# Kernel tuning notes

Hardware: AMD Instinct MI355X
Metric: run time of the kernel (lower is better)

The kernel has to match this reference:

```python
import jax, jax.numpy as jnp
import numpy as np

B, N, MODEL_D = 2, 1024, 2048
KQ_D, V_D, H, I = 128, 128, 8, 4
ROPE_THETA = 10000.0


def _rope(x, theta):
    # x: [b, n, ..., d]; positions along axis 1, rotation over last dim d.
    d = x.shape[-1]
    n = x.shape[1]
    inv_freq = theta ** (-jnp.arange(0, d, 2, dtype=jnp.float32) / d)  # [d/2]
    ang = jnp.arange(n, dtype=jnp.float32)[:, None] * inv_freq          # [n, d/2]
    bshape = (1, n) + (1,) * (x.ndim - 3) + (d // 2,)
    cos = jnp.cos(ang).reshape(bshape).astype(x.dtype)
    sin = jnp.sin(ang).reshape(bshape).astype(x.dtype)
    x1, x2 = jnp.split(x, 2, axis=-1)
    return jnp.concatenate([x1 * cos - x2 * sin, x1 * sin + x2 * cos], axis=-1)


def setup_inputs() -> dict:
    key = jax.random.key(0)
    kx, kq, kk, kv, ko = jax.random.split(key, 5)
    s_in = 1.0 / np.sqrt(MODEL_D)
    s_out = 1.0 / np.sqrt(H * I * V_D)
    x = jax.random.normal(kx, (B, N, MODEL_D), jnp.float32)
    Wq = jax.random.normal(kq, (MODEL_D, H, I, KQ_D), jnp.float32) * s_in
    Wk = jax.random.normal(kk, (MODEL_D, H, KQ_D), jnp.float32) * s_in
    Wv = jax.random.normal(kv, (MODEL_D, H, V_D), jnp.float32) * s_in
    Wo = jax.random.normal(ko, (H, I, V_D, MODEL_D), jnp.float32) * s_out
    return {"x": x, "Wq": Wq, "Wk": Wk, "Wv": Wv, "Wo": Wo}


def reference(x, Wq, Wk, Wv, Wo):
    # GQA projections (per Ueajsum specs)
    q = jnp.einsum('bnd,dhik->bnhik', x, Wq)   # [B,N,H,I,K]
    k = jnp.einsum('bnd,dhc->bnhc', x, Wk)     # [B,N,H,K]
    v = jnp.einsum('bnd,dhv->bnhv', x, Wv)     # [B,N,H,V]
    # RoPE on q and k
    q = _rope(q, ROPE_THETA)
    k = _rope(k, ROPE_THETA)
    # Causal softmax attention, each kv head serves I query heads
    scale = 1.0 / np.sqrt(KQ_D)
    scores = jnp.einsum('bnhic,bmhc->bhinm', q, k) * scale  # [B,H,I,N,N]
    n = x.shape[1]
    causal = jnp.tril(jnp.ones((n, n), dtype=bool))
    scores = jnp.where(causal, scores, jnp.finfo(scores.dtype).min)
    p = jax.nn.softmax(scores, axis=-1)
    out = jnp.einsum('bhinm,bmhv->bnhiv', p, v)              # [B,N,H,I,V]
    return jnp.einsum('bnhiv,hivd->bnd', out, Wo)            # [B,N,D]
```

## Files before the change

### kernel.cpp

```cpp
#include <hip/hip_runtime.h>
#include <hip/hip_bf16.h>

typedef __bf16 bf16x8 __attribute__((ext_vector_type(8)));
typedef float floatx4 __attribute__((ext_vector_type(4)));

static __device__ __forceinline__ void async_cp16(const __bf16* g, __bf16* l) {
    typedef const __attribute__((address_space(1))) unsigned int gu32;
    typedef __attribute__((address_space(3))) unsigned int lu32;
    __builtin_amdgcn_global_load_lds((gu32*)g, (lu32*)l, 16, 0, 0);
}

__global__ __launch_bounds__(256) void prep_kernel(
    const float* __restrict__ x,  __bf16* __restrict__ xb,
    const float* __restrict__ Wq, const float* __restrict__ Wk,
    const float* __restrict__ Wv, __bf16* __restrict__ Wt)
{
    __shared__ float tile[32][33];
    const int bk  = blockIdx.x;
    const int tid = threadIdx.x;
    const int tx  = tid & 31, ty = tid >> 5;

    if (bk < 12288) {
        const float* src; __bf16* dst; int R = 2048, C; int bxx, byy;
        if (bk < 8192)        { src = Wq; dst = Wt;                          C = 4096; bxx = bk & 127;           byy = bk >> 7; }
        else if (bk < 10240)  { src = Wk; dst = Wt + (size_t)4096 * 2048;    C = 1024; bxx = (bk - 8192) & 31;   byy = (bk - 8192) >> 5; }
        else                  { src = Wv; dst = Wt + (size_t)5120 * 2048;    C = 1024; bxx = (bk - 10240) & 31;  byy = (bk - 10240) >> 5; }
        const int c0 = bxx * 32, r0 = byy * 32;
        #pragma unroll
        for (int j = 0; j < 4; ++j)
            tile[ty * 4 + j][tx] = src[(size_t)(r0 + ty * 4 + j) * C + c0 + tx];
        __syncthreads();
        #pragma unroll
        for (int j = 0; j < 4; ++j)
            dst[(size_t)(c0 + ty * 4 + j) * R + r0 + tx] = (__bf16)tile[tx][ty * 4 + j];
    } else {
        int idx = (bk - 12288) * 256 + tid;
        const float* p = x + (size_t)idx * 8;
        float4 f0 = *(const float4*)p;
        float4 f1 = *(const float4*)(p + 4);
        union { uint4 u; __bf16 b[8]; } o;
        o.b[0] = (__bf16)f0.x; o.b[1] = (__bf16)f0.y; o.b[2] = (__bf16)f0.z; o.b[3] = (__bf16)f0.w;
        o.b[4] = (__bf16)f1.x; o.b[5] = (__bf16)f1.y; o.b[6] = (__bf16)f1.z; o.b[7] = (__bf16)f1.w;
        *(uint4*)(xb + (size_t)idx * 8) = o.u;
    }
}

__global__ void transpose_cvt_kernel(const float* __restrict__ src,
                                     __bf16* __restrict__ dst, int R, int C)
{
    __shared__ float tile[32][33];
    const int tx = threadIdx.x, ty = threadIdx.y;
    const int c0 = blockIdx.x * 32, r0 = blockIdx.y * 32;
    #pragma unroll
    for (int j = 0; j < 4; ++j)
        tile[ty * 4 + j][tx] = src[(size_t)(r0 + ty * 4 + j) * C + c0 + tx];
    __syncthreads();
    #pragma unroll
    for (int j = 0; j < 4; ++j)
        dst[(size_t)(c0 + ty * 4 + j) * R + r0 + tx] = (__bf16)tile[tx][ty * 4 + j];
}

__global__ __launch_bounds__(256) void rope_vtrans_kernel(
    __bf16* __restrict__ qkv, __bf16* __restrict__ vt)
{
    __shared__ __bf16 tile[32][33];
    const int bk  = blockIdx.x;
    const int tid = threadIdx.x;

    if (bk < 2560) {
        int idx  = bk * 256 + tid;
        int part = idx & 7;
        int t    = idx >> 3;
        int head = t % 40;
        int row  = t / 40;
        int n    = row & 1023;
        int col0 = (head < 32) ? head * 128 : 4096 + (head - 32) * 128;
        size_t base = (size_t)row * 6144 + col0 + part * 8;

        union { uint4 u; __bf16 b[8]; } x1, x2, o1, o2;
        x1.u = *(const uint4*)(qkv + base);
        x2.u = *(const uint4*)(qkv + base + 64);
        #pragma unroll
        for (int e = 0; e < 8; ++e) {
            int j = part * 8 + e;
            float inv_freq = exp2f(-(float)j * 0.20762050593046015f);
            float ang = (float)n * inv_freq;
            float sv, cv;
            __sincosf(ang, &sv, &cv);
            float a = (float)x1.b[e], b2 = (float)x2.b[e];
            o1.b[e] = (__bf16)(a * cv - b2 * sv);
            o2.b[e] = (__bf16)(a * sv + b2 * cv);
        }
        *(uint4*)(qkv + base)      = o1.u;
        *(uint4*)(qkv + base + 64) = o2.u;
    } else {
        int idx = bk - 2560;
        const int tx = tid & 31, ty = tid >> 5;
        const int k0 = (idx & 31) * 32;
        const int v0 = ((idx >> 5) & 3) * 32;
        const int bh = idx >> 7;
        const int b = bh >> 3, h = bh & 7;
        #pragma unroll
        for (int j = 0; j < 4; ++j)
            tile[ty * 4 + j][tx] =
                qkv[(size_t)(b * 1024 + k0 + ty * 4 + j) * 6144 + 5120 + h * 128 + v0 + tx];
        __syncthreads();
        #pragma unroll
        for (int j = 0; j < 4; ++j)
            vt[((size_t)bh * 128 + v0 + ty * 4 + j) * 1024 + k0 + tx] = tile[tx][ty * 4 + j];
    }
}

template <typename TC>
__global__ __launch_bounds__(256) void gemm_bt(
    const __bf16* __restrict__ A,
    const __bf16* __restrict__ Bt,
    TC* __restrict__ C,
    int M, int N, int Kc, int lda, int ldb, int ldc)
{
    __shared__ __bf16 As[128 * 32];
    __shared__ __bf16 Bs[128 * 32];

    const int tid  = threadIdx.x;
    const int wave = tid >> 6;
    const int lane = tid & 63;
    const int quad = lane >> 4;
    const int l15  = lane & 15;
    const int wr   = wave >> 1, wc = wave & 1;

    const int bm = blockIdx.y * 128;
    const int bn = blockIdx.x * 128;
    const int z  = blockIdx.z;

    A  += (size_t)z * Kc;
    Bt += (size_t)z * Kc;
    C  += (size_t)z * M * ldc;

    floatx4 acc[16];
    #pragma unroll
    for (int i = 0; i < 16; ++i) acc[i] = floatx4{0.f, 0.f, 0.f, 0.f};

    const __bf16* a0 = A  + (size_t)(bm + wave * 32 + (lane >> 2)) * lda + (lane & 3) * 8;
    const __bf16* b0 = Bt + (size_t)(bn + wave * 32 + (lane >> 2)) * ldb + (lane & 3) * 8;
    __bf16* asd0 = As + (wave * 32) * 32;
    __bf16* asd1 = As + (wave * 32 + 16) * 32;
    __bf16* bsd0 = Bs + (wave * 32) * 32;
    __bf16* bsd1 = Bs + (wave * 32 + 16) * 32;

    for (int k0 = 0; k0 < Kc; k0 += 32) {
        __syncthreads();
        async_cp16(a0 + k0,                    asd0);
        async_cp16(a0 + (size_t)16 * lda + k0, asd1);
        async_cp16(b0 + k0,                    bsd0);
        async_cp16(b0 + (size_t)16 * ldb + k0, bsd1);
        __syncthreads();

        bf16x8 af[4], bf[4];
        #pragma unroll
        for (int t = 0; t < 4; ++t)
            af[t] = *(const bf16x8*)(&As[(wr * 64 + t * 16 + l15) * 32 + quad * 8]);
        #pragma unroll
        for (int u = 0; u < 4; ++u)
            bf[u] = *(const bf16x8*)(&Bs[(wc * 64 + u * 16 + l15) * 32 + quad * 8]);
        #pragma unroll
        for (int t = 0; t < 4; ++t)
            #pragma unroll
            for (int u = 0; u < 4; ++u)
                acc[t * 4 + u] = __builtin_amdgcn_mfma_f32_16x16x32_bf16(
                    af[t], bf[u], acc[t * 4 + u], 0, 0, 0);
    }

    #pragma unroll
    for (int t = 0; t < 4; ++t)
        #pragma unroll
        for (int u = 0; u < 4; ++u)
            #pragma unroll
            for (int r = 0; r < 4; ++r) {
                int row = bm + wr * 64 + t * 16 + quad * 4 + r;
                int col = bn + wc * 64 + u * 16 + l15;
                C[(size_t)row * ldc + col] = (TC)acc[t * 4 + u][r];
            }
}

__global__ __launch_bounds__(256) void reduce_kernel(
    const __bf16* __restrict__ part, float* __restrict__ out)
{
    int idx = blockIdx.x * 256 + threadIdx.x;
    const size_t STRIDE = (size_t)2048 * 2048;
    union { uint4 u; __bf16 b[8]; } p0, p1;
    p0.u = *(const uint4*)(part + (size_t)idx * 8);
    p1.u = *(const uint4*)(part + STRIDE + (size_t)idx * 8);
    float4 o0, o1;
    o0.x = (float)p0.b[0] + (float)p1.b[0];
    o0.y = (float)p0.b[1] + (float)p1.b[1];
    o0.z = (float)p0.b[2] + (float)p1.b[2];
    o0.w = (float)p0.b[3] + (float)p1.b[3];
    o1.x = (float)p0.b[4] + (float)p1.b[4];
    o1.y = (float)p0.b[5] + (float)p1.b[5];
    o1.z = (float)p0.b[6] + (float)p1.b[6];
    o1.w = (float)p0.b[7] + (float)p1.b[7];
    *(float4*)(out + (size_t)idx * 8)     = o0;
    *(float4*)(out + (size_t)idx * 8 + 4) = o1;
}

__global__ __launch_bounds__(512, 2) void attn_kernel(
    const __bf16* __restrict__ qkv,
    const __bf16* __restrict__ vt,
    __bf16* __restrict__ ao)
{
    const int PS_LD = 72;
    __shared__ __bf16 Ks[64 * 128];
    __shared__ __bf16 Vs[128 * 64];
    __shared__ __bf16 Ps[8][16 * PS_LD];

    const int tid  = threadIdx.x;
    const int wave = tid >> 6;
    const int lane = tid & 63;
    const int quad = lane >> 4;
    const int l15  = lane & 15;
    const int i    = wave >> 1;
    const int rt   = wave & 1;

    const int pair = blockIdx.x;
    const int bh   = blockIdx.y;
    const int b    = bh >> 3, h = bh & 7;
    const __bf16* vtb = vt + (size_t)bh * 128 * 1024;

    const int keyA = wave * 8 + (lane >> 4);
    const int keyB = keyA + 4;
    const int chA  = (lane & 15) ^ (keyA & 15);
    const int chB  = (lane & 15) ^ (keyB & 15);
    const __bf16* gK0 = qkv + (size_t)(b * 1024 + keyA) * 6144 + 4096 + h * 128 + chA * 8;
    const __bf16* gK1 = qkv + (size_t)(b * 1024 + keyB) * 6144 + 4096 + h * 128 + chB * 8;
    __bf16* lK0 = Ks + (wave * 8) * 128;
    __bf16* lK1 = Ks + (wave * 8 + 4) * 128;

    const int vdA = wave * 16 + (lane >> 3);
    const int vdB = vdA + 8;
    const int cvA = (lane & 7) ^ (vdA & 7);
    const int cvB = (lane & 7) ^ (vdB & 7);
    const __bf16* gV0 = vtb + (size_t)vdA * 1024 + cvA * 8;
    const __bf16* gV1 = vtb + (size_t)vdB * 1024 + cvB * 8;
    __bf16* lV0 = Vs + (wave * 16) * 64;
    __bf16* lV1 = Vs + (wave * 16 + 8) * 64;

    bf16x8 onesf;
    #pragma unroll
    for (int j = 0; j < 8; ++j) onesf[j] = (__bf16)1.0f;

    const float C2 = 0.12751898549f;

    #pragma unroll
    for (int ph = 0; ph < 2; ++ph) {
        const int qt    = ph ? (31 - pair) : pair;
        const int qrow0 = qt * 32 + rt * 16;

        const __bf16* qp = qkv + (size_t)(b * 1024 + qrow0 + l15) * 6144 + (h * 4 + i) * 128;
        bf16x8 qf[4];
        #pragma unroll
        for (int c = 0; c < 4; ++c)
            qf[c] = *(const bf16x8*)(qp + c * 32 + quad * 8);

        floatx4 acc[8];
        #pragma unroll
        for (int u = 0; u < 8; ++u) acc[u] = floatx4{0.f, 0.f, 0.f, 0.f};
        floatx4 accl = floatx4{0.f, 0.f, 0.f, 0.f};

        const int ntiles = (qt >> 1) + 1;
        for (int t = 0; t < ntiles; ++t) {
            const int kt = t * 64;
            __syncthreads();
            async_cp16(gK0 + (size_t)kt * 6144, lK0);
            async_cp16(gK1 + (size_t)kt * 6144, lK1);
            async_cp16(gV0 + kt, lV0);
            async_cp16(gV1 + kt, lV1);
            __syncthreads();

            floatx4 s[4];
            #pragma unroll
            for (int ks = 0; ks < 4; ++ks) s[ks] = floatx4{0.f, 0.f, 0.f, 0.f};
            #pragma unroll
            for (int c = 0; c < 4; ++c) {
                #pragma unroll
                for (int ks = 0; ks < 4; ++ks) {
                    bf16x8 kf = *(const bf16x8*)(
                        &Ks[(ks * 16 + l15) * 128 + ((c * 4 + quad) ^ l15) * 8]);
                    s[ks] = __builtin_amdgcn_mfma_f32_16x16x32_bf16(qf[c], kf, s[ks], 0, 0, 0);
                }
            }

            #pragma unroll
            for (int r = 0; r < 4; ++r) {
                int qrow = qrow0 + quad * 4 + r;
                #pragma unroll
                for (int ks = 0; ks < 4; ++ks) {
                    int kc = kt + ks * 16 + l15;
                    float p = (kc <= qrow) ? exp2f(s[ks][r] * C2) : 0.0f;
                    Ps[wave][(quad * 4 + r) * PS_LD + ks * 16 + l15] = (__bf16)p;
                }
            }

            #pragma unroll
            for (int s2 = 0; s2 < 2; ++s2) {
                bf16x8 pa = *(const bf16x8*)(&Ps[wave][l15 * PS_LD + s2 * 32 + quad * 8]);
                accl = __builtin_amdgcn_mfma_f32_16x16x32_bf16(pa, onesf, accl, 0, 0, 0);
                #pragma unroll
                for (int u = 0; u < 8; ++u) {
                    bf16x8 vf = *(const bf16x8*)(
                        &Vs[(u * 16 + l15) * 64 + (((s2 * 4 + quad) ^ (l15 & 7))) * 8]);
                    acc[u] = __builtin_amdgcn_mfma_f32_16x16x32_bf16(pa, vf, acc[u], 0, 0, 0);
                }
            }
        }

        #pragma unroll
        for (int r = 0; r < 4; ++r) {
            float inv = 1.0f / accl[r];
            int row = qrow0 + quad * 4 + r;
            __bf16* op = ao + (size_t)(b * 1024 + row) * 4096 + (h * 4 + i) * 128;
            #pragma unroll
            for (int u = 0; u < 8; ++u)
                op[u * 16 + l15] = (__bf16)(acc[u][r] * inv);
        }
    }
}

extern "C" void kernel_launch(void* const* d_in, const int* in_sizes, int n_in,
                              void* d_out, int out_size, void* d_ws, size_t ws_size,
                              hipStream_t stream)
{
    const float* x  = (const float*)d_in[0];
    const float* Wq = (const float*)d_in[1];
    const float* Wk = (const float*)d_in[2];
    const float* Wv = (const float*)d_in[3];
    const float* Wo = (const float*)d_in[4];
    float* out = (float*)d_out;

    const size_t MB = 1024 * 1024;
    char* ws = (char*)d_ws;
    __bf16* qkv  = (__bf16*)(ws);
    __bf16* vtb  = (__bf16*)(ws + 24 * MB);
    __bf16* xb   = (__bf16*)(ws + 28 * MB);
    __bf16* Wt   = (__bf16*)(ws + 36 * MB);
    __bf16* ao   = (__bf16*)(ws + 28 * MB);
    __bf16* WoT  = (__bf16*)(ws + 44 * MB);
    __bf16* part = (__bf16*)(ws);

    prep_kernel<<<14336, 256, 0, stream>>>(x, xb, Wq, Wk, Wv, Wt);
    gemm_bt<__bf16><<<dim3(48, 16), 256, 0, stream>>>(xb, Wt, qkv, 2048, 6144, 2048, 2048, 2048, 6144);
    transpose_cvt_kernel<<<dim3(64, 128), dim3(32, 8), 0, stream>>>(Wo, WoT, 4096, 2048);
    rope_vtrans_kernel<<<4608, 256, 0, stream>>>(qkv, vtb);
    attn_kernel<<<dim3(16, 16), 512, 0, stream>>>(qkv, vtb, ao);
    gemm_bt<__bf16><<<dim3(16, 16, 2), 256, 0, stream>>>(ao, WoT, part, 2048, 2048, 2048, 4096, 4096, 2048);
    reduce_kernel<<<2048, 256, 0, stream>>>(part, out);
}
```

Before: 323.5 us.

## Use swizzled 64-wide K tiles in GEMM, 3-way split-K, fuse Wo transpose

The GEMM now stages 64-wide K slices per sync, using an XOR swizzle on LDS columns to avoid bank conflicts. This halves the number of barrier pairs per K and doubles the MFMA work per load phase. The output projection switches from a 2-way to an uneven 3-way split-K (1344/1344/1408) for more blocks and better CU occupancy, with the reduce kernel summing three partials. The Wo transpose/convert is folded into the rope/V-transpose launch to remove one kernel launch. LDS use per block doubles, and the extra partial adds memory traffic in the reduce step.

```diff
diff --git a/kernel.cpp b/kernel.cpp
--- a/kernel.cpp
+++ b/kernel.cpp
@@ -45,25 +45,12 @@
     }
 }
 
-__global__ void transpose_cvt_kernel(const float* __restrict__ src,
-                                     __bf16* __restrict__ dst, int R, int C)
-{
-    __shared__ float tile[32][33];
-    const int tx = threadIdx.x, ty = threadIdx.y;
-    const int c0 = blockIdx.x * 32, r0 = blockIdx.y * 32;
-    #pragma unroll
-    for (int j = 0; j < 4; ++j)
-        tile[ty * 4 + j][tx] = src[(size_t)(r0 + ty * 4 + j) * C + c0 + tx];
-    __syncthreads();
-    #pragma unroll
-    for (int j = 0; j < 4; ++j)
-        dst[(size_t)(c0 + ty * 4 + j) * R + r0 + tx] = (__bf16)tile[tx][ty * 4 + j];
-}
-
-__global__ __launch_bounds__(256) void rope_vtrans_kernel(
-    __bf16* __restrict__ qkv, __bf16* __restrict__ vt)
-{
-    __shared__ __bf16 tile[32][33];
+__global__ __launch_bounds__(256) void rope_vtrans_wot_kernel(
+    __bf16* __restrict__ qkv, __bf16* __restrict__ vt,
+    const float* __restrict__ Wo, __bf16* __restrict__ WoT)
+{
+    __shared__ float tilef[32][33];
+    __shared__ __bf16 tileb[32][33];
     const int bk  = blockIdx.x;
     const int tid = threadIdx.x;
 
@@ -93,7 +80,7 @@
         }
         *(uint4*)(qkv + base)      = o1.u;
         *(uint4*)(qkv + base + 64) = o2.u;
-    } else {
+    } else if (bk < 4608) {
         int idx = bk - 2560;
         const int tx = tid & 31, ty = tid >> 5;
         const int k0 = (idx & 31) * 32;
@@ -102,24 +89,36 @@
         const int b = bh >> 3, h = bh & 7;
         #pragma unroll
         for (int j = 0; j < 4; ++j)
-            tile[ty * 4 + j][tx] =
+            tileb[ty * 4 + j][tx] =
                 qkv[(size_t)(b * 1024 + k0 + ty * 4 + j) * 6144 + 5120 + h * 128 + v0 + tx];
         __syncthreads();
         #pragma unroll
         for (int j = 0; j < 4; ++j)
-            vt[((size_t)bh * 128 + v0 + ty * 4 + j) * 1024 + k0 + tx] = tile[tx][ty * 4 + j];
+            vt[((size_t)bh * 128 + v0 + ty * 4 + j) * 1024 + k0 + tx] = tileb[tx][ty * 4 + j];
+    } else {
+        int idx = bk - 4608;
+        const int tx = tid & 31, ty = tid >> 5;
+        const int c0 = (idx & 63) * 32;
+        const int r0 = (idx >> 6) * 32;
+        #pragma unroll
+        for (int j = 0; j < 4; ++j)
+            tilef[ty * 4 + j][tx] = Wo[(size_t)(r0 + ty * 4 + j) * 2048 + c0 + tx];
+        __syncthreads();
+        #pragma unroll
+        for (int j = 0; j < 4; ++j)
+            WoT[(size_t)(c0 + ty * 4 + j) * 4096 + r0 + tx] = (__bf16)tilef[tx][ty * 4 + j];
     }
 }
 
-template <typename TC>
 __global__ __launch_bounds__(256) void gemm_bt(
     const __bf16* __restrict__ A,
     const __bf16* __restrict__ Bt,
-    TC* __restrict__ C,
-    int M, int N, int Kc, int lda, int ldb, int ldc)
-{
-    __shared__ __bf16 As[128 * 32];
-    __shared__ __bf16 Bs[128 * 32];
+    __bf16* __restrict__ C,
+    int M, int lda, int ldb, int ldc,
+    int kc_base, int kc_extra)
+{
+    __shared__ __bf16 As[128 * 64];
+    __shared__ __bf16 Bs[128 * 64];
 
     const int tid  = threadIdx.x;
     const int wave = tid >> 6;
@@ -131,43 +130,50 @@
     const int bm = blockIdx.y * 128;
     const int bn = blockIdx.x * 128;
     const int z  = blockIdx.z;
-
-    A  += (size_t)z * Kc;
-    Bt += (size_t)z * Kc;
+    const int Kc = kc_base + ((z == (int)gridDim.z - 1) ? kc_extra : 0);
+
+    A  += (size_t)z * kc_base;
+    Bt += (size_t)z * kc_base;
     C  += (size_t)z * M * ldc;
 
     floatx4 acc[16];
     #pragma unroll
     for (int i = 0; i < 16; ++i) acc[i] = floatx4{0.f, 0.f, 0.f, 0.f};
 
-    const __bf16* a0 = A  + (size_t)(bm + wave * 32 + (lane >> 2)) * lda + (lane & 3) * 8;
-    const __bf16* b0 = Bt + (size_t)(bn + wave * 32 + (lane >> 2)) * ldb + (lane & 3) * 8;
-    __bf16* asd0 = As + (wave * 32) * 32;
-    __bf16* asd1 = As + (wave * 32 + 16) * 32;
-    __bf16* bsd0 = Bs + (wave * 32) * 32;
-    __bf16* bsd1 = Bs + (wave * 32 + 16) * 32;
-
-    for (int k0 = 0; k0 < Kc; k0 += 32) {
-        __syncthreads();
-        async_cp16(a0 + k0,                    asd0);
-        async_cp16(a0 + (size_t)16 * lda + k0, asd1);
-        async_cp16(b0 + k0,                    bsd0);
-        async_cp16(b0 + (size_t)16 * ldb + k0, bsd1);
-        __syncthreads();
-
-        bf16x8 af[4], bf[4];
-        #pragma unroll
-        for (int t = 0; t < 4; ++t)
-            af[t] = *(const bf16x8*)(&As[(wr * 64 + t * 16 + l15) * 32 + quad * 8]);
-        #pragma unroll
-        for (int u = 0; u < 4; ++u)
-            bf[u] = *(const bf16x8*)(&Bs[(wc * 64 + u * 16 + l15) * 32 + quad * 8]);
-        #pragma unroll
-        for (int t = 0; t < 4; ++t)
+    const int sr = lane >> 3;
+    const int sc = ((lane & 7) ^ sr) * 8;
+    const __bf16* a0 = A  + (size_t)(bm + wave * 32 + sr) * lda + sc;
+    const __bf16* b0 = Bt + (size_t)(bn + wave * 32 + sr) * ldb + sc;
+    __bf16* asd = As + (wave * 32) * 64;
+    __bf16* bsd = Bs + (wave * 32) * 64;
+
+    for (int k0 = 0; k0 < Kc; k0 += 64) {
+        __syncthreads();
+        #pragma unroll
+        for (int r = 0; r < 4; ++r) {
+            async_cp16(a0 + (size_t)(r * 8) * lda + k0, asd + (r * 8) * 64);
+            async_cp16(b0 + (size_t)(r * 8) * ldb + k0, bsd + (r * 8) * 64);
+        }
+        __syncthreads();
+
+        #pragma unroll
+        for (int ko = 0; ko < 2; ++ko) {
+            bf16x8 af[4], bf[4];
+            #pragma unroll
+            for (int t = 0; t < 4; ++t)
+                af[t] = *(const bf16x8*)(
+                    &As[(wr * 64 + t * 16 + l15) * 64 + (((ko * 4 + quad) ^ (l15 & 7)) * 8)]);
             #pragma unroll
             for (int u = 0; u < 4; ++u)
-                acc[t * 4 + u] = __builtin_amdgcn_mfma_f32_16x16x32_bf16(
-                    af[t], bf[u], acc[t * 4 + u], 0, 0, 0);
+                bf[u] = *(const bf16x8*)(
+                    &Bs[(wc * 64 + u * 16 + l15) * 64 + (((ko * 4 + quad) ^ (l15 & 7)) * 8)]);
+            #pragma unroll
+            for (int t = 0; t < 4; ++t)
+                #pragma unroll
+                for (int u = 0; u < 4; ++u)
+                    acc[t * 4 + u] = __builtin_amdgcn_mfma_f32_16x16x32_bf16(
+                        af[t], bf[u], acc[t * 4 + u], 0, 0, 0);
+        }
     }
 
     #pragma unroll
@@ -178,7 +184,7 @@
             for (int r = 0; r < 4; ++r) {
                 int row = bm + wr * 64 + t * 16 + quad * 4 + r;
                 int col = bn + wc * 64 + u * 16 + l15;
-                C[(size_t)row * ldc + col] = (TC)acc[t * 4 + u][r];
+                C[(size_t)row * ldc + col] = (__bf16)acc[t * 4 + u][r];
             }
 }
 
@@ -186,19 +192,20 @@
     const __bf16* __restrict__ part, float* __restrict__ out)
 {
     int idx = blockIdx.x * 256 + threadIdx.x;
-    const size_t STRIDE = (size_t)2048 * 2048;
-    union { uint4 u; __bf16 b[8]; } p0, p1;
+    const size_t S = (size_t)2048 * 2048;
+    union { uint4 u; __bf16 b[8]; } p0, p1, p2;
     p0.u = *(const uint4*)(part + (size_t)idx * 8);
-    p1.u = *(const uint4*)(part + STRIDE + (size_t)idx * 8);
+    p1.u = *(const uint4*)(part + S + (size_t)idx * 8);
+    p2.u = *(const uint4*)(part + 2 * S + (size_t)idx * 8);
     float4 o0, o1;
-    o0.x = (float)p0.b[0] + (float)p1.b[0];
-    o0.y = (float)p0.b[1] + (float)p1.b[1];
-    o0.z = (float)p0.b[2] + (float)p1.b[2];
-    o0.w = (float)p0.b[3] + (float)p1.b[3];
-    o1.x = (float)p0.b[4] + (float)p1.b[4];
-    o1.y = (float)p0.b[5] + (float)p1.b[5];
-    o1.z = (float)p0.b[6] + (float)p1.b[6];
-    o1.w = (float)p0.b[7] + (float)p1.b[7];
+    o0.x = (float)p0.b[0] + (float)p1.b[0] + (float)p2.b[0];
+    o0.y = (float)p0.b[1] + (float)p1.b[1] + (float)p2.b[1];
+    o0.z = (float)p0.b[2] + (float)p1.b[2] + (float)p2.b[2];
+    o0.w = (float)p0.b[3] + (float)p1.b[3] + (float)p2.b[3];
+    o1.x = (float)p0.b[4] + (float)p1.b[4] + (float)p2.b[4];
+    o1.y = (float)p0.b[5] + (float)p1.b[5] + (float)p2.b[5];
+    o1.z = (float)p0.b[6] + (float)p1.b[6] + (float)p2.b[6];
+    o1.w = (float)p0.b[7] + (float)p1.b[7] + (float)p2.b[7];
     *(float4*)(out + (size_t)idx * 8)     = o0;
     *(float4*)(out + (size_t)idx * 8 + 4) = o1;
 }
@@ -342,15 +349,14 @@
     __bf16* vtb  = (__bf16*)(ws + 24 * MB);
     __bf16* xb   = (__bf16*)(ws + 28 * MB);
     __bf16* Wt   = (__bf16*)(ws + 36 * MB);
-    __bf16* ao   = (__bf16*)(ws + 28 * MB);
-    __bf16* WoT  = (__bf16*)(ws + 44 * MB);
+    __bf16* WoT  = (__bf16*)(ws + 28 * MB);
+    __bf16* ao   = (__bf16*)(ws + 44 * MB);
     __bf16* part = (__bf16*)(ws);
 
     prep_kernel<<<14336, 256, 0, stream>>>(x, xb, Wq, Wk, Wv, Wt);
-    gemm_bt<__bf16><<<dim3(48, 16), 256, 0, stream>>>(xb, Wt, qkv, 2048, 6144, 2048, 2048, 2048, 6144);
-    transpose_cvt_kernel<<<dim3(64, 128), dim3(32, 8), 0, stream>>>(Wo, WoT, 4096, 2048);
-    rope_vtrans_kernel<<<4608, 256, 0, stream>>>(qkv, vtb);
+    gemm_bt<<<dim3(48, 16), 256, 0, stream>>>(xb, Wt, qkv, 2048, 2048, 2048, 6144, 2048, 0);
+    rope_vtrans_wot_kernel<<<12800, 256, 0, stream>>>(qkv, vtb, Wo, WoT);
     attn_kernel<<<dim3(16, 16), 512, 0, stream>>>(qkv, vtb, ao);
-    gemm_bt<__bf16><<<dim3(16, 16, 2), 256, 0, stream>>>(ao, WoT, part, 2048, 2048, 2048, 4096, 4096, 2048);
+    gemm_bt<<<dim3(16, 16, 3), 256, 0, stream>>>(ao, WoT, part, 2048, 4096, 4096, 2048, 1344, 64);
     reduce_kernel<<<2048, 256, 0, stream>>>(part, out);
 }
```

Result: faster. 300.3 us (-7.2%).
